# Performance work log

Measured on AMD Instinct MI355X. Metric: run time of the kernel, lower is better.

The kernel has to match this reference:

```python
import jax, jax.numpy as jnp
import numpy as np

EMBED_DIM = 1024
NUM_HEADS = 16
HEAD_DIM = EMBED_DIM // NUM_HEADS
SCALING = HEAD_DIM ** -0.5


def setup_inputs() -> dict:
    key = jax.random.key(0)
    k1, k2, k3, k4, k5 = jax.random.split(key, 5)
    B, S, E, H = 2, 2048, EMBED_DIM, NUM_HEADS
    x = jax.random.normal(k1, (B, S, E), dtype=jnp.float32)
    # nn.Linear weights: [out_features, in_features]
    W_A = jax.random.normal(k2, (H, E), dtype=jnp.float32) * (E ** -0.5)
    W_V = jax.random.normal(k3, (E, E), dtype=jnp.float32) * (E ** -0.5)
    W_O = jax.random.normal(k4, (E, E), dtype=jnp.float32) * (E ** -0.5)
    b_O = jax.random.normal(k5, (E,), dtype=jnp.float32) * 0.01
    return {"x": x, "W_A": W_A, "W_V": W_V, "W_O": W_O, "b_O": b_O}


def reference(x, W_A, W_V, W_O, b_O):
    B, S, E = x.shape
    H, D = NUM_HEADS, HEAD_DIM
    # per-head scalar attention logits, softmax over sequence dim
    z = jnp.einsum('bse,he->bsh', x, W_A) * SCALING          # [B,S,H]
    z = jax.nn.softmax(z, axis=1)                            # softmax over seq
    zp = jnp.transpose(z, (0, 2, 1))                         # [B,H,S]
    # causal roll matrix: roll[b,h,i,j] = z[b,h,i-j] for j<=i else 0
    i = jnp.arange(S)[:, None]
    j = jnp.arange(S)[None, :]
    idx = (i - j) % S                                        # [S,S]
    tril = (j <= i).astype(x.dtype)                          # causal mask
    roll = zp[:, :, idx] * tril                              # [B,H,S,S]
    # values split into heads
    v = jnp.einsum('bse,fe->bsf', x, W_V).reshape(B, S, H, D)  # [B,S,H,D]
    out = jnp.einsum('bhij,bjhd->bihd', roll, v).reshape(B, S, E)
    return jnp.einsum('bse,fe->bsf', out, W_O) + b_O
```

## Files before the change

kernel.cpp:

```cpp
#include <hip/hip_runtime.h>
#include <hip/hip_bf16.h>
#include <stdint.h>

typedef unsigned short u16;
typedef short short8 __attribute__((ext_vector_type(8)));
typedef float f32x4 __attribute__((ext_vector_type(4)));

#define SEQ 2048
#define EMB 1024
#define NH 16
#define HD 64
#define ZP 2112

__device__ inline u16 f2bf(float f) {
    uint32_t u = __builtin_bit_cast(uint32_t, f);
    uint32_t r = (u + 0x7FFFu + ((u >> 16) & 1u)) >> 16;
    return (u16)r;
}

__device__ inline void gload16(const void* g, void* l) {
    __builtin_amdgcn_global_load_lds(
        (const __attribute__((address_space(1))) void*)g,
        (__attribute__((address_space(3))) void*)l, 16, 0, 0);
}

__global__ __launch_bounds__(256) void cast_logits(const float* __restrict__ x,
                                                   const float* __restrict__ W_A,
                                                   const float* __restrict__ W_V,
                                                   const float* __restrict__ W_O,
                                                   u16* __restrict__ xb,
                                                   u16* __restrict__ wvb,
                                                   u16* __restrict__ wob,
                                                   float* __restrict__ zl) {
    const int bid = blockIdx.x, t = threadIdx.x;
    if (bid >= 256) {
        int j = (bid - 256) * 256 + t;
        const float* src;
        u16* dst;
        if (j < 262144) { src = W_V; dst = wvb; }
        else { j -= 262144; src = W_O; dst = wob; }
        float4 f = reinterpret_cast<const float4*>(src)[j];
        union { u16 u[4]; uint2 v; } o;
        o.u[0] = f2bf(f.x); o.u[1] = f2bf(f.y); o.u[2] = f2bf(f.z); o.u[3] = f2bf(f.w);
        reinterpret_cast<uint2*>(dst)[j] = o.v;
        return;
    }
    __shared__ float wa[NH * EMB];
    for (int i = t; i < NH * EMB / 4; i += 256)
        reinterpret_cast<float4*>(wa)[i] = reinterpret_cast<const float4*>(W_A)[i];
    __syncthreads();
    const int w = t >> 6, l = t & 63;
    const int row0 = bid * 16 + w * 4;
    for (int rr = 0; rr < 4; rr++) {
        int gs = row0 + rr;
        int b = gs >> 11, s = gs & 2047;
        const float* xr = x + (size_t)gs * EMB;
        float xv[16];
#pragma unroll
        for (int q = 0; q < 16; q++) xv[q] = xr[l + 64 * q];
        u16* xw = xb + (size_t)gs * EMB;
#pragma unroll
        for (int q = 0; q < 16; q++) xw[l + 64 * q] = f2bf(xv[q]);
#pragma unroll
        for (int h = 0; h < NH; h++) {
            float a = 0.f;
#pragma unroll
            for (int q = 0; q < 16; q++) a += xv[q] * wa[h * EMB + l + 64 * q];
#pragma unroll
            for (int off = 32; off; off >>= 1) a += __shfl_xor(a, off);
            if (l == h) zl[((size_t)b * NH + h) * SEQ + s] = a * 0.125f;
        }
    }
}

__device__ void softmax_body(const float* __restrict__ zl, u16* __restrict__ zr, int bh) {
    const float* src = zl + (size_t)bh * SEQ;
    int t = threadIdx.x;
    int w = t >> 6, l = t & 63;
    __shared__ float red4[4];
    __shared__ float bc;
    float v[8];
#pragma unroll
    for (int q = 0; q < 8; q++) v[q] = src[t + 256 * q];
    float m = v[0];
#pragma unroll
    for (int q = 1; q < 8; q++) m = fmaxf(m, v[q]);
#pragma unroll
    for (int off = 32; off; off >>= 1) m = fmaxf(m, __shfl_xor(m, off));
    if (l == 0) red4[w] = m;
    __syncthreads();
    if (t == 0) bc = fmaxf(fmaxf(red4[0], red4[1]), fmaxf(red4[2], red4[3]));
    __syncthreads();
    m = bc;
    float s = 0.f;
#pragma unroll
    for (int q = 0; q < 8; q++) { v[q] = expf(v[q] - m); s += v[q]; }
#pragma unroll
    for (int off = 32; off; off >>= 1) s += __shfl_xor(s, off);
    if (l == 0) red4[w] = s;
    __syncthreads();
    if (t == 0) bc = red4[0] + red4[1] + red4[2] + red4[3];
    __syncthreads();
    float inv = 1.0f / bc;
#pragma unroll
    for (int q = 0; q < 8; q++) {
        int sidx = t + 256 * q;
        zr[(size_t)bh * ZP + (SEQ - 1 - sidx)] = f2bf(v[q] * inv);
    }
    if (t < ZP - SEQ) zr[(size_t)bh * ZP + SEQ + t] = 0;
}

template <int OUTMODE, int MAP, bool SM>
__global__ __launch_bounds__(256) void gemm64(const u16* __restrict__ A,
                                              const u16* __restrict__ Bw,
                                              u16* __restrict__ Cb, float* __restrict__ Cf,
                                              const float* __restrict__ bias,
                                              int M, int N, int K,
                                              const float* __restrict__ zl,
                                              u16* __restrict__ zr) {
    if constexpr (SM) {
        if (blockIdx.x >= 512) { softmax_body(zl, zr, blockIdx.x - 512); return; }
    }
    __shared__ u16 As[2][128 * 64];
    __shared__ u16 Bs[2][64 * 64];
    const int t = threadIdx.x;
    const int i = blockIdx.x;
    int xg, yg;
    if constexpr (MAP == 0) { xg = (i & 7) * 8 + ((i >> 3) & 7); yg = i >> 6; }
    else                    { yg = (i & 7) * 4 + ((i >> 3) & 3); xg = i >> 5; }
    const int m0 = yg * 128, n0 = xg * 64;
    const int w = t >> 6, l = t & 63;
    const int wr = w >> 1, wc = w & 1;
    const int lrow = l & 15, lk = l >> 4;
    const int r7 = lrow & 7;

    const int srow = t >> 3;
    const int scb = ((t & 7) ^ ((t >> 3) & 7)) * 8;
    const u16* gA = A + (size_t)(m0 + srow) * K + scb;
    const u16* gB = Bw + (size_t)(n0 + srow) * K + scb;
    const int ldst = w * 512;

    f32x4 acc[4][2];
#pragma unroll
    for (int a = 0; a < 4; a++)
#pragma unroll
        for (int b = 0; b < 2; b++) acc[a][b] = (f32x4){0.f, 0.f, 0.f, 0.f};

    const int NT = K >> 6;
    const size_t rk32 = (size_t)32 * K;
#pragma unroll
    for (int c = 0; c < 4; c++) gload16(gA + c * rk32, &As[0][ldst + 2048 * c]);
#pragma unroll
    for (int c = 0; c < 2; c++) gload16(gB + c * rk32, &Bs[0][ldst + 2048 * c]);
    __syncthreads();

    for (int kt = 0; kt < NT; kt++) {
        const int cur = kt & 1;
        if (kt + 1 < NT) {
            const int k0 = (kt + 1) * 64;
#pragma unroll
            for (int c = 0; c < 4; c++) gload16(gA + k0 + c * rk32, &As[cur ^ 1][ldst + 2048 * c]);
#pragma unroll
            for (int c = 0; c < 2; c++) gload16(gB + k0 + c * rk32, &Bs[cur ^ 1][ldst + 2048 * c]);
        }
#pragma unroll
        for (int kk = 0; kk < 2; kk++) {
            const int cs = ((kk * 4 + lk) ^ r7) * 8;
            short8 af[4], bf2[2];
#pragma unroll
            for (int mi = 0; mi < 4; mi++)
                af[mi] = *reinterpret_cast<const short8*>(
                    &As[cur][(wr * 64 + mi * 16 + lrow) * 64 + cs]);
#pragma unroll
            for (int ni = 0; ni < 2; ni++)
                bf2[ni] = *reinterpret_cast<const short8*>(
                    &Bs[cur][(wc * 32 + ni * 16 + lrow) * 64 + cs]);
#pragma unroll
            for (int mi = 0; mi < 4; mi++)
#pragma unroll
                for (int ni = 0; ni < 2; ni++)
                    acc[mi][ni] = __builtin_amdgcn_mfma_f32_16x16x32_bf16(af[mi], bf2[ni], acc[mi][ni], 0, 0, 0);
        }
        __syncthreads();
    }
#pragma unroll
    for (int mi = 0; mi < 4; mi++)
#pragma unroll
        for (int ni = 0; ni < 2; ni++)
#pragma unroll
            for (int r = 0; r < 4; r++) {
                int row = m0 + wr * 64 + mi * 16 + lk * 4 + r;
                int col = n0 + wc * 32 + ni * 16 + lrow;
                if constexpr (OUTMODE == 0)
                    Cb[(size_t)row * N + col] = f2bf(acc[mi][ni][r]);
                else
                    Cf[(size_t)row * N + col] = acc[mi][ni][r] + bias[col];
            }
}

__global__ __launch_bounds__(256) void conv2(const u16* __restrict__ zr,
                                             const u16* __restrict__ vt2,
                                             u16* __restrict__ cv) {
    const int i = blockIdx.x;
    const int bh = (i & 7) * 4 + ((i >> 3) & 3);
    const int rest = i >> 5;
    const int ch = rest & 1;
    const int gsel = rest >> 1;
    const int b = bh >> 4, h = bh & 15;
    __shared__ uint zsl[2176];
    __shared__ u16 Bt[2][32 * 64];
    const int t = threadIdx.x;
    {
        const uint* zp = reinterpret_cast<const uint*>(zr + (size_t)bh * ZP);
        for (int q = t; q < 1088; q += 256) {
            uint v0 = (q < 1056) ? zp[q] : 0u;
            uint v1 = (q < 1055) ? zp[q + 1] : 0u;
            zsl[q] = v0;
            zsl[1088 + q] = (v0 >> 16) | (v1 << 16);
        }
    }
    const int w = t >> 6, l = t & 63;
    const int lrow = l & 15, lk = l >> 4, lk8 = lk * 8;
    const int ebase = h * 64 + ch * 32;
    const size_t boff = (size_t)b * SEQ;

    const int rB = w * 8 + (l >> 3);
    const int Csrc = (l & 7) ^ (rB & 7);
    const u16* gB = vt2 + (((size_t)(ebase + rB)) << 12) + boff + Csrc * 8;
    const int dbase = w * 512;
    __syncthreads();

    union U { uint d[4]; short8 s8; };
    const int gms[2] = {gsel, 7 - gsel};
#pragma unroll 1
    for (int si = 0; si < 2; si++) {
        const int gm = gms[si];
        const int kend = (gm + 1) * 256;
        const int ns = kend >> 6;
        const int r0 = gm * 256 + w * 64;
        const int wkmax = r0 + 64;
        const int obase0 = 2047 - r0 - lrow + lk8;
        f32x4 acc[4][2];
#pragma unroll
        for (int a = 0; a < 4; a++)
#pragma unroll
            for (int c = 0; c < 2; c++) acc[a][c] = (f32x4){0.f, 0.f, 0.f, 0.f};

        gload16(gB, &Bt[0][dbase]);
        for (int s = 0; s < ns; s++) {
            const int cur = s & 1;
            const int k0 = s * 64;
            if (s + 1 < ns) gload16(gB + k0 + 64, &Bt[cur ^ 1][dbase]);
            __syncthreads();
            if (k0 < wkmax) {
#pragma unroll
                for (int kk = 0; kk < 2; kk++) {
                    U af[4];
                    short8 bf2[2];
#pragma unroll
                    for (int mi = 0; mi < 4; mi++) {
                        int o = obase0 - mi * 16 + k0 + kk * 32;
                        uint adw = (uint)(o >> 1) + (uint)((o & 1) * 1088);
#pragma unroll
                        for (int q = 0; q < 4; q++) af[mi].d[q] = zsl[adw + q];
                    }
#pragma unroll
                    for (int ni = 0; ni < 2; ni++) {
                        int row = ni * 16 + lrow;
                        int c2 = (((kk * 4 + lk) ^ (row & 7))) * 8;
                        bf2[ni] = *reinterpret_cast<const short8*>(&Bt[cur][row * 64 + c2]);
                    }
#pragma unroll
                    for (int mi = 0; mi < 4; mi++)
#pragma unroll
                        for (int ni = 0; ni < 2; ni++)
                            acc[mi][ni] = __builtin_amdgcn_mfma_f32_16x16x32_bf16(af[mi].s8, bf2[ni], acc[mi][ni], 0, 0, 0);
                }
            }
            __syncthreads();
        }
#pragma unroll
        for (int mi = 0; mi < 4; mi++)
#pragma unroll
            for (int ni = 0; ni < 2; ni++)
#pragma unroll
                for (int rr = 0; rr < 4; rr++) {
                    int row = r0 + mi * 16 + lk * 4 + rr;
                    int col = ebase + ni * 16 + lrow;
                    cv[((size_t)b * SEQ + row) * EMB + col] = f2bf(acc[mi][ni][rr]);
                }
    }
}

extern "C" void kernel_launch(void* const* d_in, const int* in_sizes, int n_in,
                              void* d_out, int out_size, void* d_ws, size_t ws_size,
                              hipStream_t stream) {
    const float* x   = (const float*)d_in[0];
    const float* W_A = (const float*)d_in[1];
    const float* W_V = (const float*)d_in[2];
    const float* W_O = (const float*)d_in[3];
    const float* b_O = (const float*)d_in[4];

    char* ws = (char*)d_ws;
    u16*   xb  = (u16*)(ws + 0);
    u16*   wvb = (u16*)(ws + 8388608);
    u16*   wob = (u16*)(ws + 10485760);
    float* zl  = (float*)(ws + 12582912);
    u16*   zr  = (u16*)(ws + 12845056);
    u16*   vt2 = (u16*)(ws + 12980224);
    u16*   cv  = (u16*)(ws + 21368832);

    cast_logits<<<2304, 256, 0, stream>>>(x, W_A, W_V, W_O, xb, wvb, wob, zl);
    gemm64<0, 0, true><<<544, 256, 0, stream>>>(wvb, xb, vt2, nullptr, nullptr,
                                                1024, 4096, 1024, zl, zr);
    conv2<<<256, 256, 0, stream>>>(zr, vt2, cv);
    gemm64<1, 1, false><<<512, 256, 0, stream>>>(cv, wob, nullptr, (float*)d_out, b_O,
                                                 4096, 1024, 1024, nullptr, nullptr);
}
```

Measured before the change: 99.89 us.

## Replace LDS-staged GEMM with single-wave register-direct 64x64 tiles

The shared-memory double-buffered 128x64 GEMM with four waves per block is replaced by a one-wave 64x64 tile kernel. Each wave loads MFMA fragments straight from global memory into registers, using a two-stage software prefetch, and drops all LDS traffic and block barriers. The fused softmax is reworked to run in a single 64-thread wave with shuffle-only reductions. The aim is to remove LDS and sync overhead and launch twice as many blocks. In exchange, each tile's operands are fetched from global memory without sharing between waves, so L2 traffic rises and loads are less coalesced.

Measured after the change: 132.4 us. +32.6%, slower.

```diff
diff --git a/kernel.cpp b/kernel.cpp
--- a/kernel.cpp
+++ b/kernel.cpp
@@ -73,45 +73,31 @@
     }
 }
 
-__device__ void softmax_body(const float* __restrict__ zl, u16* __restrict__ zr, int bh) {
+__device__ void softmax64(const float* __restrict__ zl, u16* __restrict__ zr, int bh) {
     const float* src = zl + (size_t)bh * SEQ;
-    int t = threadIdx.x;
-    int w = t >> 6, l = t & 63;
-    __shared__ float red4[4];
-    __shared__ float bc;
-    float v[8];
-#pragma unroll
-    for (int q = 0; q < 8; q++) v[q] = src[t + 256 * q];
+    const int l = threadIdx.x;
+    float v[32];
+#pragma unroll
+    for (int q = 0; q < 32; q++) v[q] = src[l + 64 * q];
     float m = v[0];
 #pragma unroll
-    for (int q = 1; q < 8; q++) m = fmaxf(m, v[q]);
+    for (int q = 1; q < 32; q++) m = fmaxf(m, v[q]);
 #pragma unroll
     for (int off = 32; off; off >>= 1) m = fmaxf(m, __shfl_xor(m, off));
-    if (l == 0) red4[w] = m;
-    __syncthreads();
-    if (t == 0) bc = fmaxf(fmaxf(red4[0], red4[1]), fmaxf(red4[2], red4[3]));
-    __syncthreads();
-    m = bc;
     float s = 0.f;
 #pragma unroll
-    for (int q = 0; q < 8; q++) { v[q] = expf(v[q] - m); s += v[q]; }
+    for (int q = 0; q < 32; q++) { v[q] = expf(v[q] - m); s += v[q]; }
 #pragma unroll
     for (int off = 32; off; off >>= 1) s += __shfl_xor(s, off);
-    if (l == 0) red4[w] = s;
-    __syncthreads();
-    if (t == 0) bc = red4[0] + red4[1] + red4[2] + red4[3];
-    __syncthreads();
-    float inv = 1.0f / bc;
-#pragma unroll
-    for (int q = 0; q < 8; q++) {
-        int sidx = t + 256 * q;
-        zr[(size_t)bh * ZP + (SEQ - 1 - sidx)] = f2bf(v[q] * inv);
-    }
-    if (t < ZP - SEQ) zr[(size_t)bh * ZP + SEQ + t] = 0;
+    float inv = 1.0f / s;
+#pragma unroll
+    for (int q = 0; q < 32; q++)
+        zr[(size_t)bh * ZP + (SEQ - 1 - (l + 64 * q))] = f2bf(v[q] * inv);
+    zr[(size_t)bh * ZP + SEQ + l] = 0;
 }
 
 template <int OUTMODE, int MAP, bool SM>
-__global__ __launch_bounds__(256) void gemm64(const u16* __restrict__ A,
+__global__ __launch_bounds__(64) void gemm_rw(const u16* __restrict__ A,
                                               const u16* __restrict__ Bw,
                                               u16* __restrict__ Cb, float* __restrict__ Cf,
                                               const float* __restrict__ bias,
@@ -119,78 +105,70 @@
                                               const float* __restrict__ zl,
                                               u16* __restrict__ zr) {
     if constexpr (SM) {
-        if (blockIdx.x >= 512) { softmax_body(zl, zr, blockIdx.x - 512); return; }
-    }
-    __shared__ u16 As[2][128 * 64];
-    __shared__ u16 Bs[2][64 * 64];
-    const int t = threadIdx.x;
+        if (blockIdx.x >= 1024) { softmax64(zl, zr, blockIdx.x - 1024); return; }
+    }
     const int i = blockIdx.x;
+    const int xcd = i & 7, idx = i >> 3;
+    const int many = (idx >> 4) * 8 + xcd;
+    const int few = idx & 15;
     int xg, yg;
-    if constexpr (MAP == 0) { xg = (i & 7) * 8 + ((i >> 3) & 7); yg = i >> 6; }
-    else                    { yg = (i & 7) * 4 + ((i >> 3) & 3); xg = i >> 5; }
-    const int m0 = yg * 128, n0 = xg * 64;
-    const int w = t >> 6, l = t & 63;
-    const int wr = w >> 1, wc = w & 1;
-    const int lrow = l & 15, lk = l >> 4;
-    const int r7 = lrow & 7;
-
-    const int srow = t >> 3;
-    const int scb = ((t & 7) ^ ((t >> 3) & 7)) * 8;
-    const u16* gA = A + (size_t)(m0 + srow) * K + scb;
-    const u16* gB = Bw + (size_t)(n0 + srow) * K + scb;
-    const int ldst = w * 512;
-
-    f32x4 acc[4][2];
+    if constexpr (MAP == 0) { xg = many; yg = few; }
+    else                    { yg = many; xg = few; }
+    const int m0 = yg * 64, n0 = xg * 64;
+    const int l = threadIdx.x;
+    const int lrow = l & 15, lk = l >> 4, lk8 = lk * 8;
+
+    const u16* pA[4];
+    const u16* pB[4];
+#pragma unroll
+    for (int q = 0; q < 4; q++) {
+        pA[q] = A + (size_t)(m0 + q * 16 + lrow) * K + lk8;
+        pB[q] = Bw + (size_t)(n0 + q * 16 + lrow) * K + lk8;
+    }
+
+    f32x4 acc[4][4];
 #pragma unroll
     for (int a = 0; a < 4; a++)
 #pragma unroll
-        for (int b = 0; b < 2; b++) acc[a][b] = (f32x4){0.f, 0.f, 0.f, 0.f};
-
-    const int NT = K >> 6;
-    const size_t rk32 = (size_t)32 * K;
-#pragma unroll
-    for (int c = 0; c < 4; c++) gload16(gA + c * rk32, &As[0][ldst + 2048 * c]);
-#pragma unroll
-    for (int c = 0; c < 2; c++) gload16(gB + c * rk32, &Bs[0][ldst + 2048 * c]);
-    __syncthreads();
-
-    for (int kt = 0; kt < NT; kt++) {
-        const int cur = kt & 1;
-        if (kt + 1 < NT) {
-            const int k0 = (kt + 1) * 64;
-#pragma unroll
-            for (int c = 0; c < 4; c++) gload16(gA + k0 + c * rk32, &As[cur ^ 1][ldst + 2048 * c]);
-#pragma unroll
-            for (int c = 0; c < 2; c++) gload16(gB + k0 + c * rk32, &Bs[cur ^ 1][ldst + 2048 * c]);
-        }
-#pragma unroll
-        for (int kk = 0; kk < 2; kk++) {
-            const int cs = ((kk * 4 + lk) ^ r7) * 8;
-            short8 af[4], bf2[2];
-#pragma unroll
-            for (int mi = 0; mi < 4; mi++)
-                af[mi] = *reinterpret_cast<const short8*>(
-                    &As[cur][(wr * 64 + mi * 16 + lrow) * 64 + cs]);
-#pragma unroll
-            for (int ni = 0; ni < 2; ni++)
-                bf2[ni] = *reinterpret_cast<const short8*>(
-                    &Bs[cur][(wc * 32 + ni * 16 + lrow) * 64 + cs]);
-#pragma unroll
-            for (int mi = 0; mi < 4; mi++)
-#pragma unroll
-                for (int ni = 0; ni < 2; ni++)
-                    acc[mi][ni] = __builtin_amdgcn_mfma_f32_16x16x32_bf16(af[mi], bf2[ni], acc[mi][ni], 0, 0, 0);
-        }
-        __syncthreads();
-    }
+        for (int b = 0; b < 4; b++) acc[a][b] = (f32x4){0.f, 0.f, 0.f, 0.f};
+
+    union U { uint4 v; short8 s8; };
+    U a0[4], b0[4], a1[4], b1[4];
+
+    auto LD = [&](int k0, U* af, U* bf) {
+#pragma unroll
+        for (int q = 0; q < 4; q++) af[q].v = *reinterpret_cast<const uint4*>(pA[q] + k0);
+#pragma unroll
+        for (int q = 0; q < 4; q++) bf[q].v = *reinterpret_cast<const uint4*>(pB[q] + k0);
+    };
+    auto MM = [&](U* af, U* bf) {
+#pragma unroll
+        for (int mi = 0; mi < 4; mi++)
+#pragma unroll
+            for (int ni = 0; ni < 4; ni++)
+                acc[mi][ni] = __builtin_amdgcn_mfma_f32_16x16x32_bf16(af[mi].s8, bf[ni].s8, acc[mi][ni], 0, 0, 0);
+    };
+
+    LD(0, a0, b0);
+    LD(32, a1, b1);
+#pragma unroll 1
+    for (int k0 = 0; k0 < K - 64; k0 += 64) {
+        MM(a0, b0);
+        LD(k0 + 64, a0, b0);
+        MM(a1, b1);
+        if (k0 + 96 < K) LD(k0 + 96, a1, b1);
+    }
+    MM(a0, b0);
+    MM(a1, b1);
+
 #pragma unroll
     for (int mi = 0; mi < 4; mi++)
 #pragma unroll
-        for (int ni = 0; ni < 2; ni++)
+        for (int ni = 0; ni < 4; ni++)
 #pragma unroll
             for (int r = 0; r < 4; r++) {
-                int row = m0 + wr * 64 + mi * 16 + lk * 4 + r;
-                int col = n0 + wc * 32 + ni * 16 + lrow;
+                int row = m0 + mi * 16 + lk * 4 + r;
+                int col = n0 + ni * 16 + lrow;
                 if constexpr (OUTMODE == 0)
                     Cb[(size_t)row * N + col] = f2bf(acc[mi][ni][r]);
                 else
@@ -311,9 +289,9 @@
     u16*   cv  = (u16*)(ws + 21368832);
 
     cast_logits<<<2304, 256, 0, stream>>>(x, W_A, W_V, W_O, xb, wvb, wob, zl);
-    gemm64<0, 0, true><<<544, 256, 0, stream>>>(wvb, xb, vt2, nullptr, nullptr,
-                                                1024, 4096, 1024, zl, zr);
+    gemm_rw<0, 0, true><<<1056, 64, 0, stream>>>(wvb, xb, vt2, nullptr, nullptr,
+                                                 1024, 4096, 1024, zl, zr);
     conv2<<<256, 256, 0, stream>>>(zr, vt2, cv);
-    gemm64<1, 1, false><<<512, 256, 0, stream>>>(cv, wob, nullptr, (float*)d_out, b_O,
-                                                 4096, 1024, 1024, nullptr, nullptr);
-}
+    gemm_rw<1, 1, false><<<1024, 64, 0, stream>>>(cv, wob, nullptr, (float*)d_out, b_O,
+                                                  4096, 1024, 1024, nullptr, nullptr);
+}
```
